# Optimization experiments

Hardware: AMD Instinct MI355X
Metric: run time of the kernel (lower is better)

## Reference

```python
import jax, jax.numpy as jnp
import numpy as np

T, B, E = 2048, 2, 1024
H, R = 16, 8
HD = E // H          # head_dim = 64
VD = E // R          # value_dim = attn_dim // num_rules = 128 (attn_dim = embed_dim)
SEL = E // H         # selection_dim = 64


def _linear_params(key, out_dim, in_dim):
    kw, kb = jax.random.split(key)
    lim = float(np.sqrt(6.0 / (in_dim + out_dim)))  # xavier_uniform
    W = jax.random.uniform(kw, (out_dim, in_dim), jnp.float32, -lim, lim)
    b = jnp.zeros((out_dim,), jnp.float32)
    return W, b


def setup_inputs() -> dict:
    key = jax.random.key(0)
    ks = jax.random.split(key, 7)
    query = jax.random.normal(ks[0], (T, B, E), jnp.float32)
    Wq, bq = _linear_params(ks[1], E, E)
    Wk, bk = _linear_params(ks[2], E, E)
    Wv, bv = _linear_params(ks[3], E, E)          # v_proj: embed_dim -> attn_dim (=E)
    Wvq, bvq = _linear_params(ks[4], SEL * H, E)  # value_q (q_compose=False)
    Wsc, bsc = _linear_params(ks[5], 1, SEL + VD) # score_network (nonlinear=False)
    Wo, bo = _linear_params(ks[6], E, H * VD)     # out_proj
    return {"query": query, "Wq": Wq, "bq": bq, "Wk": Wk, "bk": bk,
            "Wv": Wv, "bv": bv, "Wvq": Wvq, "bvq": bvq,
            "Wsc": Wsc, "bsc": bsc, "Wo": Wo, "bo": bo}


def reference(query, Wq, bq, Wk, bk, Wv, bv, Wvq, bvq, Wsc, bsc, Wo, bo):
    t, b, e = query.shape
    scaling = HD ** -0.5
    # projections (self-attention: k, v from query)
    q = (query @ Wq.T + bq) * scaling                       # (T,B,E)
    k = query @ Wk.T + bk                                   # (T,B,E)
    v = query @ Wv.T + bv                                   # (T,B,attn_dim)
    q = q.reshape(t, b, H, HD).transpose(1, 2, 0, 3)        # (B,H,T,HD)
    k = k.reshape(t, b, H, HD).transpose(1, 2, 0, 3)        # (B,H,S,HD)
    v = v.reshape(t, b, R, VD).transpose(1, 2, 0, 3)        # (B,R,S,VD)
    # standard multi-head search: softmax over source positions
    probs = jax.nn.softmax(jnp.einsum('bhtd,bhsd->bhts', q, k), axis=-1)
    # per-(head, rule) retrieved values
    attn = jnp.einsum('bhts,brsd->bhtrd', probs, v)         # (B,H,T,R,VD)
    # selection query from raw input (q_compose=False)
    v_q = (query @ Wvq.T + bvq).reshape(t, b, H, SEL).transpose(1, 2, 0, 3)  # (B,H,T,SEL)
    v_q = jnp.broadcast_to(v_q[:, :, :, None, :], (b, H, t, R, SEL))
    comp = jnp.concatenate([v_q, attn], axis=-1)            # (B,H,T,R,SEL+VD)
    score = comp @ Wsc.T + bsc                              # (B,H,T,R,1)
    sel = jax.nn.softmax(score, axis=3)                     # softmax over rules
    out = jnp.sum(attn * sel, axis=3)                       # (B,H,T,VD)
    out = out.transpose(2, 0, 1, 3).reshape(t, b, H * VD)   # (T,B,H*VD)
    return out @ Wo.T + bo                                  # (T,B,E)
```

## Files before the change

kernel.cpp:

```cpp
#include <hip/hip_runtime.h>
#include <hip/hip_bf16.h>
#include <stdint.h>

typedef unsigned short u16;
typedef unsigned int u32;
typedef __attribute__((ext_vector_type(8))) short bf16x8;
typedef __attribute__((ext_vector_type(4))) float f32x4;

#define TT 2048
#define BB 2
#define HH 16
#define RR 8
#define SS 2048
#define MROWS 4096

__device__ __forceinline__ float bf2f(u16 h){ union { u32 u; float f; } v; v.u = ((u32)h) << 16; return v.f; }
__device__ __forceinline__ u16 f2bf(float f){ union { float f; u32 u; } v; v.f = f; return (u16)((v.u + 0x7FFFu + ((v.u >> 16) & 1u)) >> 16); }
__device__ __forceinline__ void gl_lds16(const void* g, void* l){
  __builtin_amdgcn_global_load_lds((const __attribute__((address_space(1))) u32*)g,
                                   (__attribute__((address_space(3))) u32*)l, 16, 0, 0);
}

__global__ void k_cvt(const float* __restrict__ s, u16* __restrict__ d, int n, float scale){
  int i = blockIdx.x * blockDim.x + threadIdx.x;
  int st = gridDim.x * blockDim.x;
  for (; i < n; i += st) d[i] = f2bf(s[i] * scale);
}

__global__ void k_bias(const float* __restrict__ bq, const float* __restrict__ bk,
                       const float* __restrict__ bv, float* __restrict__ bb){
  int i = blockIdx.x * blockDim.x + threadIdx.x;
  if (i < 1024){ bb[i] = bq[i] * 0.125f; bb[1024 + i] = bk[i]; bb[2048 + i] = bv[i]; }
}

template<int KD, bool OBF>
__launch_bounds__(256, 2)
__global__ void k_gemm(const u16* __restrict__ A, const u16* __restrict__ Bt,
                       const float* __restrict__ bias, void* __restrict__ Cout, int ldc){
  __shared__ u16 As[128*32];
  __shared__ u16 Bs[128*32];
  const int tid = threadIdx.x, lane = tid & 63, wid = tid >> 6;
  const int mw = wid >> 1, nw = wid & 1;
  const int m0 = blockIdx.y * 128, n0 = blockIdx.x * 128;
  const f32x4 fzero = {0.f, 0.f, 0.f, 0.f};
  f32x4 acc[4][4];
  #pragma unroll
  for (int a = 0; a < 4; ++a)
    #pragma unroll
    for (int c = 0; c < 4; ++c) acc[a][c] = fzero;

  for (int k0 = 0; k0 < KD; k0 += 32){
    #pragma unroll
    for (int it = 0; it < 2; ++it){
      int c = it*256 + tid, r = c >> 2, sl = c & 3;
      gl_lds16(A + (size_t)(m0 + r)*KD + k0 + 8*(sl ^ ((r >> 1) & 3)), &As[c*8]);
    }
    #pragma unroll
    for (int it = 0; it < 2; ++it){
      int c = it*256 + tid, r = c >> 2, sl = c & 3;
      gl_lds16(Bt + (size_t)(n0 + r)*KD + k0 + 8*(sl ^ ((r >> 1) & 3)), &Bs[c*8]);
    }
    __syncthreads();
    bf16x8 af[4], bfr[4];
    #pragma unroll
    for (int mt = 0; mt < 4; ++mt){
      int r = mw*64 + mt*16 + (lane & 15);
      int pos = (lane >> 4) ^ ((r >> 1) & 3);
      af[mt] = *(const bf16x8*)&As[r*32 + pos*8];
    }
    #pragma unroll
    for (int nt = 0; nt < 4; ++nt){
      int r = nw*64 + nt*16 + (lane & 15);
      int pos = (lane >> 4) ^ ((r >> 1) & 3);
      bfr[nt] = *(const bf16x8*)&Bs[r*32 + pos*8];
    }
    #pragma unroll
    for (int mt = 0; mt < 4; ++mt)
      #pragma unroll
      for (int nt = 0; nt < 4; ++nt)
        acc[mt][nt] = __builtin_amdgcn_mfma_f32_16x16x32_bf16(af[mt], bfr[nt], acc[mt][nt], 0, 0, 0);
    __syncthreads();
  }
  #pragma unroll
  for (int nt = 0; nt < 4; ++nt){
    int col = n0 + nw*64 + nt*16 + (lane & 15);
    float bvv = bias[col];
    #pragma unroll
    for (int mt = 0; mt < 4; ++mt)
      #pragma unroll
      for (int j = 0; j < 4; ++j){
        int row = m0 + mw*64 + mt*16 + (lane >> 4)*4 + j;
        float v = acc[mt][nt][j] + bvv;
        if constexpr (OBF) ((u16*)Cout)[(size_t)row*ldc + col] = f2bf(v);
        else               ((float*)Cout)[(size_t)row*ldc + col] = v;
      }
  }
}

__global__ void k_transpose(const u16* __restrict__ qkvb, u16* __restrict__ Vt2){
  __shared__ u16 tile[32][33];
  const int b = blockIdx.z;
  const int s0 = blockIdx.x * 32, n0 = blockIdx.y * 32;
  const int tx = threadIdx.x & 31, ty = threadIdx.x >> 5;
  for (int i = ty; i < 32; i += 8)
    tile[i][tx] = qkvb[(size_t)((s0 + i)*BB + b)*3072 + 2048 + n0 + tx];
  __syncthreads();
  for (int i = ty; i < 32; i += 8){
    int c = n0 + i;
    int nr = ((c & 127) << 3) | (c >> 7);
    Vt2[(size_t)b*1024*SS + (size_t)nr*SS + s0 + tx] = tile[tx][i];
  }
}

__global__ void k_vw2(const u16* __restrict__ qkvb, const float* __restrict__ Wsc,
                      u16* __restrict__ vwa){
  int idx = blockIdx.x * blockDim.x + threadIdx.x;
  if (idx >= BB*16*SS) return;
  int s = idx & (SS - 1);
  int r = (idx >> 11) & 15;
  int b = idx >> 15;
  float a;
  if (r < 8){
    const u16* vrow = qkvb + (size_t)(s*BB + b)*3072 + 2048 + r*128;
    a = 0.f;
    #pragma unroll 8
    for (int d = 0; d < 128; ++d) a += bf2f(vrow[d]) * Wsc[64 + d];
  } else if (r == 8) a = 1.0f;
  else a = 0.f;
  vwa[(size_t)(b*16 + r)*SS + s] = f2bf(a);
}

__launch_bounds__(512, 4)
__global__ void k_attn2(const u16* __restrict__ qkvb, const u16* __restrict__ vwa,
                        u16* __restrict__ probs, float* __restrict__ selp, int bh0){
  __shared__ u16 Qs[64*64];
  __shared__ u16 Ks[128*64];
  __shared__ u16 P[64*136];
  __shared__ float pwL[8][16][16];
  const int tid = threadIdx.x, lane = tid & 63, wid = tid >> 6;
  const int bhl = blockIdx.y;
  const int bh = bh0 + bhl;
  const int t0 = blockIdx.x * 64;
  const int b = bh >> 4, h = bh & 15;
  const u16* qbase = qkvb + b*3072 + h*64;
  const u16* kbase = qkvb + b*3072 + 1024 + h*64;
  const u16* vwbase = vwa + (size_t)b*16*SS;
  u16* pbase = probs + ((size_t)bhl*TT + t0)*SS;
  const f32x4 fzero = {0.f, 0.f, 0.f, 0.f};

  {
    int c = tid, r = c >> 3, sl = c & 7;
    gl_lds16(qbase + (size_t)(t0 + r)*6144 + 8*(sl ^ (r & 7)), &Qs[c*8]);
  }
  __syncthreads();
  bf16x8 qf[4][2];
  #pragma unroll
  for (int mt = 0; mt < 4; ++mt)
    #pragma unroll
    for (int kk = 0; kk < 2; ++kk){
      int r = mt*16 + (lane & 15);
      int pos = (kk*4 + (lane >> 4)) ^ (r & 7);
      qf[mt][kk] = *(const bf16x8*)&Qs[r*64 + pos*8];
    }

  f32x4 pwacc = fzero;
  const int mtp = wid & 3, kks = (wid >> 2)*2;

  for (int s0 = 0; s0 < SS; s0 += 128){
    #pragma unroll
    for (int it = 0; it < 2; ++it){
      int c = it*512 + tid, r = c >> 3, sl = c & 7;
      gl_lds16(kbase + (size_t)(s0 + r)*6144 + 8*(sl ^ (r & 7)), &Ks[c*8]);
    }
    __syncthreads();
    bf16x8 kf[2];
    #pragma unroll
    for (int kk = 0; kk < 2; ++kk){
      int r = wid*16 + (lane & 15);
      int pos = (kk*4 + (lane >> 4)) ^ (r & 7);
      kf[kk] = *(const bf16x8*)&Ks[r*64 + pos*8];
    }
    #pragma unroll
    for (int bt = 0; bt < 4; ++bt){
      f32x4 sa = fzero;
      sa = __builtin_amdgcn_mfma_f32_16x16x32_bf16(kf[0], qf[bt][0], sa, 0, 0, 0);
      sa = __builtin_amdgcn_mfma_f32_16x16x32_bf16(kf[1], qf[bt][1], sa, 0, 0, 0);
      u32 w0 = (u32)f2bf(__expf(sa[0])) | ((u32)f2bf(__expf(sa[1])) << 16);
      u32 w1 = (u32)f2bf(__expf(sa[2])) | ((u32)f2bf(__expf(sa[3])) << 16);
      int t = bt*16 + (lane & 15);
      int sl = wid*16 + (lane >> 4)*4;
      uint2 pk; pk.x = w0; pk.y = w1;
      *(uint2*)&P[t*136 + sl] = pk;
    }
    __syncthreads();
    bf16x8 vwf[2];
    #pragma unroll
    for (int kq = 0; kq < 2; ++kq)
      vwf[kq] = *(const bf16x8*)&vwbase[(size_t)(lane & 15)*SS + s0 + (kks + kq)*32 + (lane >> 4)*8];
    #pragma unroll
    for (int kq = 0; kq < 2; ++kq){
      int kk = kks + kq;
      bf16x8 pa = *(const bf16x8*)&P[(mtp*16 + (lane & 15))*136 + kk*32 + (lane >> 4)*8];
      pwacc = __builtin_amdgcn_mfma_f32_16x16x32_bf16(pa, vwf[kq], pwacc, 0, 0, 0);
    }
    #pragma unroll
    for (int cc = 0; cc < 2; ++cc){
      int c = cc*512 + tid;
      int row = c >> 4, col = c & 15;
      bf16x8 v = *(const bf16x8*)&P[row*136 + col*8];
      *(bf16x8*)&pbase[(size_t)row*SS + s0 + col*8] = v;
    }
  }

  #pragma unroll
  for (int j = 0; j < 4; ++j)
    pwL[wid][(lane >> 4)*4 + j][lane & 15] = pwacc[j];
  __syncthreads();
  if (tid < 64){
    int mt = tid >> 4, tr = tid & 15;
    float pw[9];
    #pragma unroll
    for (int r = 0; r < 9; ++r) pw[r] = pwL[mt][tr][r] + pwL[mt + 4][tr][r];
    float rs = pw[8];
    float inv = 1.0f / rs;
    float mx = -3.0e38f;
    #pragma unroll
    for (int r = 0; r < 8; ++r) mx = fmaxf(mx, pw[r]*inv);
    float e[8], ssum = 0.f;
    #pragma unroll
    for (int r = 0; r < 8; ++r){ e[r] = __expf(pw[r]*inv - mx); ssum += e[r]; }
    #pragma unroll
    for (int r = 0; r < 8; ++r)
      selp[((size_t)bh*TT + t0 + tid)*8 + r] = e[r] / (ssum * rs);
  }
}

__launch_bounds__(512, 2)
__global__ void k_pv4(const u16* __restrict__ probs, const u16* __restrict__ Vt2,
                      const float* __restrict__ selp, u16* __restrict__ oattn,
                      int bh0, int G){
  __shared__ u16 L[4*16384];
  const int tid = threadIdx.x, lane = tid & 63, wid = tid >> 6;
  const int mw = wid & 1, nw2 = wid >> 1;
  int fid = blockIdx.x, bhl, xy;
  if (G >= 8){ bhl = (fid & 7) + 8*(fid >> 8); xy = (fid >> 3) & 31; }
  else       { bhl = fid >> 5;                 xy = fid & 31; }
  const int t0 = (xy >> 2) * 256;
  const int n0 = (xy & 3) * 256;
  const int bh = bh0 + bhl, b = bh >> 4, h = bh & 15;
  const u16* Abase = probs + ((size_t)bhl*TT + t0)*SS;
  const u16* Bbase = Vt2 + (size_t)b*1024*SS + (size_t)n0*SS;
  const f32x4 fzero = {0.f, 0.f, 0.f, 0.f};
  f32x4 acc[8][4];
  #pragma unroll
  for (int a = 0; a < 8; ++a)
    #pragma unroll
    for (int c = 0; c < 4; ++c) acc[a][c] = fzero;

  auto stage = [&](int q){
    u16* As = &L[(q & 3) * 16384];
    u16* Bs = As + 8192;
    #pragma unroll
    for (int i = 0; i < 2; ++i){
      int ci = i*512 + tid, r = ci >> 2, sl = ci & 3;
      gl_lds16(Abase + (size_t)r*SS + q*32 + 8*(sl ^ ((r >> 1) & 3)), &As[ci*8]);
    }
    #pragma unroll
    for (int i = 0; i < 2; ++i){
      int ci = i*512 + tid, r = ci >> 2, sl = ci & 3;
      gl_lds16(Bbase + (size_t)r*SS + q*32 + 8*(sl ^ ((r >> 1) & 3)), &Bs[ci*8]);
    }
  };

  stage(0); stage(1); stage(2);
  asm volatile("s_waitcnt vmcnt(8)" ::: "memory");
  __builtin_amdgcn_s_barrier();
  __builtin_amdgcn_sched_barrier(0);

  for (int q = 0; q < 64; ++q){
    const u16* As = &L[(q & 3) * 16384];
    const u16* Bs = As + 8192;
    bf16x8 af[8], bfr[4];
    #pragma unroll
    for (int mf = 0; mf < 8; ++mf){
      int r = mw*128 + mf*16 + (lane & 15);
      int pos = (lane >> 4) ^ ((r >> 1) & 3);
      af[mf] = *(const bf16x8*)&As[r*32 + pos*8];
    }
    #pragma unroll
    for (int nf = 0; nf < 4; ++nf){
      int r = nw2*64 + nf*16 + (lane & 15);
      int pos = (lane >> 4) ^ ((r >> 1) & 3);
      bfr[nf] = *(const bf16x8*)&Bs[r*32 + pos*8];
    }
    if (q + 3 < 64) stage(q + 3);
    __builtin_amdgcn_s_setprio(1);
    #pragma unroll
    for (int mf = 0; mf < 8; ++mf)
      #pragma unroll
      for (int nf = 0; nf < 4; ++nf)
        acc[mf][nf] = __builtin_amdgcn_mfma_f32_16x16x32_bf16(af[mf], bfr[nf], acc[mf][nf], 0, 0, 0);
    __builtin_amdgcn_s_setprio(0);
    if (q < 61)       asm volatile("s_waitcnt vmcnt(8)" ::: "memory");
    else if (q == 61) asm volatile("s_waitcnt vmcnt(4)" ::: "memory");
    else              asm volatile("s_waitcnt vmcnt(0)" ::: "memory");
    __builtin_amdgcn_s_barrier();
    __builtin_amdgcn_sched_barrier(0);
  }

  const int c15 = lane & 15, g = lane >> 4, r8 = c15 & 7;
  float sel[8][4];
  #pragma unroll
  for (int mf = 0; mf < 8; ++mf)
    #pragma unroll
    for (int j = 0; j < 4; ++j){
      int trow = t0 + mw*128 + mf*16 + g*4 + j;
      sel[mf][j] = selp[((size_t)bh*TT + trow)*8 + r8];
    }
  #pragma unroll
  for (int mf = 0; mf < 8; ++mf)
    #pragma unroll
    for (int nf = 0; nf < 4; ++nf){
      float v0 = acc[mf][nf][0] * sel[mf][0];
      float v1 = acc[mf][nf][1] * sel[mf][1];
      float v2 = acc[mf][nf][2] * sel[mf][2];
      float v3 = acc[mf][nf][3] * sel[mf][3];
      #pragma unroll
      for (int mask = 1; mask < 8; mask <<= 1){
        v0 += __shfl_xor(v0, mask, 64);
        v1 += __shfl_xor(v1, mask, 64);
        v2 += __shfl_xor(v2, mask, 64);
        v3 += __shfl_xor(v3, mask, 64);
      }
      if (r8 == 0){
        int dglob = (n0 >> 3) + nw2*8 + nf*2 + (c15 >> 3);
        int tb = t0 + mw*128 + mf*16 + g*4;
        u16* dst = oattn + (size_t)(tb*BB + b)*2048 + h*128 + dglob;
        dst[0*BB*2048] = f2bf(v0);
        dst[1*BB*2048] = f2bf(v1);
        dst[2*BB*2048] = f2bf(v2);
        dst[3*BB*2048] = f2bf(v3);
      }
    }
}

extern "C" void kernel_launch(void* const* d_in, const int* in_sizes, int n_in,
                              void* d_out, int out_size, void* d_ws, size_t ws_size,
                              hipStream_t stream){
  (void)in_sizes; (void)n_in;
  const float* query = (const float*)d_in[0];
  const float* Wq  = (const float*)d_in[1];
  const float* bq  = (const float*)d_in[2];
  const float* Wk  = (const float*)d_in[3];
  const float* bk  = (const float*)d_in[4];
  const float* Wv  = (const float*)d_in[5];
  const float* bv  = (const float*)d_in[6];
  const float* Wsc = (const float*)d_in[9];
  const float* Wo  = (const float*)d_in[11];
  const float* bo  = (const float*)d_in[12];

  char* p = (char*)d_ws;
  auto carve = [&](size_t bytes) -> char* {
    char* r = p; p += (bytes + 255) & ~((size_t)255); return r;
  };
  u16*   Xb     = (u16*)  carve((size_t)MROWS*1024*2);
  u16*   Wb     = (u16*)  carve((size_t)3072*1024*2);
  u16*   Wob    = (u16*)  carve((size_t)1024*2048*2);
  float* bb     = (float*)carve(3072*4);
  u16*   qkvb   = (u16*)  carve((size_t)MROWS*3072*2);
  u16*   Vt2    = (u16*)  carve((size_t)BB*1024*SS*2);
  u16*   vwa    = (u16*)  carve((size_t)BB*16*SS*2);
  u16*   oattn  = (u16*)  carve((size_t)MROWS*2048*2);
  float* selp   = (float*)carve((size_t)32*TT*RR*4);
  size_t fixed = (size_t)(p - (char*)d_ws);
  int G = 32;
  while (G > 1 && fixed + ((size_t)G*TT*SS*2 + 256) > ws_size) G >>= 1;
  u16* probs;
  if (fixed + ((size_t)G*TT*SS*2 + 256) <= ws_size){
    probs = (u16*)carve((size_t)G*TT*SS*2);
  } else {
    G = 1;
    probs = Xb;
  }

  k_cvt<<<1024, 256, 0, stream>>>(query, Xb, MROWS*1024, 1.0f);
  k_cvt<<<512, 256, 0, stream>>>(Wq, Wb, 1024*1024, 0.125f);
  k_cvt<<<512, 256, 0, stream>>>(Wk, Wb + 1024*1024, 1024*1024, 1.0f);
  k_cvt<<<512, 256, 0, stream>>>(Wv, Wb + 2*1024*1024, 1024*1024, 1.0f);
  k_cvt<<<1024, 256, 0, stream>>>(Wo, Wob, 1024*2048, 1.0f);
  k_bias<<<4, 256, 0, stream>>>(bq, bk, bv, bb);
  k_gemm<1024, true><<<dim3(24, 32), 256, 0, stream>>>(Xb, Wb, bb, qkvb, 3072);
  k_transpose<<<dim3(64, 32, 2), 256, 0, stream>>>(qkvb, Vt2);
  k_vw2<<<256, 256, 0, stream>>>(qkvb, Wsc, vwa);
  for (int bh0 = 0; bh0 < 32; bh0 += G){
    k_attn2<<<dim3(32, G), 512, 0, stream>>>(qkvb, vwa, probs, selp, bh0);
    k_pv4<<<G*32, 512, 0, stream>>>(probs, Vt2, selp, oattn, bh0, G);
  }
  k_gemm<2048, false><<<dim3(8, 32), 256, 0, stream>>>(oattn, Wob, bo, d_out, 1024);
}
```

Measured before the change: 433.5 us.

## Shrink PV GEMM tile to 256x128 and double-buffer LDS fragment reads

The probs×V kernel's per-block output tile shrinks from 256x256 to 256x128, doubling the grid and halving the per-wave accumulator footprint. The eight waves are regrouped as a 4x2 grid with 64x64 subtiles. Fragment reads for the next k-step are issued before the MFMAs of the current one, giving a software-pipelined A/B register double buffer. The intent is better occupancy and latency hiding, at the cost of loading each probs tile twice across N-blocks, which doubles A-operand traffic.

```diff
diff --git a/kernel.cpp b/kernel.cpp
--- a/kernel.cpp
+++ b/kernel.cpp
@@ -236,89 +236,101 @@
 }
 
 __launch_bounds__(512, 2)
-__global__ void k_pv4(const u16* __restrict__ probs, const u16* __restrict__ Vt2,
+__global__ void k_pv5(const u16* __restrict__ probs, const u16* __restrict__ Vt2,
                       const float* __restrict__ selp, u16* __restrict__ oattn,
                       int bh0, int G){
-  __shared__ u16 L[4*16384];
+  __shared__ u16 L[4*12288];
   const int tid = threadIdx.x, lane = tid & 63, wid = tid >> 6;
-  const int mw = wid & 1, nw2 = wid >> 1;
+  const int mw = wid >> 1, nw = wid & 1;
   int fid = blockIdx.x, bhl, xy;
-  if (G >= 8){ bhl = (fid & 7) + 8*(fid >> 8); xy = (fid >> 3) & 31; }
-  else       { bhl = fid >> 5;                 xy = fid & 31; }
-  const int t0 = (xy >> 2) * 256;
-  const int n0 = (xy & 3) * 256;
+  if (G >= 8){ bhl = (fid & 7) + 8*(fid >> 9); xy = (fid >> 3) & 63; }
+  else       { bhl = fid >> 6;                 xy = fid & 63; }
+  const int t0 = (xy >> 3) * 256;
+  const int n0 = (xy & 7) * 128;
   const int bh = bh0 + bhl, b = bh >> 4, h = bh & 15;
   const u16* Abase = probs + ((size_t)bhl*TT + t0)*SS;
   const u16* Bbase = Vt2 + (size_t)b*1024*SS + (size_t)n0*SS;
   const f32x4 fzero = {0.f, 0.f, 0.f, 0.f};
-  f32x4 acc[8][4];
-  #pragma unroll
-  for (int a = 0; a < 8; ++a)
+  f32x4 acc[4][4];
+  #pragma unroll
+  for (int a = 0; a < 4; ++a)
     #pragma unroll
     for (int c = 0; c < 4; ++c) acc[a][c] = fzero;
 
   auto stage = [&](int q){
-    u16* As = &L[(q & 3) * 16384];
+    u16* As = &L[(q & 3) * 12288];
     u16* Bs = As + 8192;
     #pragma unroll
     for (int i = 0; i < 2; ++i){
       int ci = i*512 + tid, r = ci >> 2, sl = ci & 3;
       gl_lds16(Abase + (size_t)r*SS + q*32 + 8*(sl ^ ((r >> 1) & 3)), &As[ci*8]);
     }
-    #pragma unroll
-    for (int i = 0; i < 2; ++i){
-      int ci = i*512 + tid, r = ci >> 2, sl = ci & 3;
+    {
+      int ci = tid, r = ci >> 2, sl = ci & 3;
       gl_lds16(Bbase + (size_t)r*SS + q*32 + 8*(sl ^ ((r >> 1) & 3)), &Bs[ci*8]);
     }
   };
-
-  stage(0); stage(1); stage(2);
-  asm volatile("s_waitcnt vmcnt(8)" ::: "memory");
-  __builtin_amdgcn_s_barrier();
-  __builtin_amdgcn_sched_barrier(0);
-
-  for (int q = 0; q < 64; ++q){
-    const u16* As = &L[(q & 3) * 16384];
+  auto read_frags = [&](int q, bf16x8 (&af)[4], bf16x8 (&bfr)[4]){
+    const u16* As = &L[(q & 3) * 12288];
     const u16* Bs = As + 8192;
-    bf16x8 af[8], bfr[4];
-    #pragma unroll
-    for (int mf = 0; mf < 8; ++mf){
-      int r = mw*128 + mf*16 + (lane & 15);
+    #pragma unroll
+    for (int mf = 0; mf < 4; ++mf){
+      int r = mw*64 + mf*16 + (lane & 15);
       int pos = (lane >> 4) ^ ((r >> 1) & 3);
       af[mf] = *(const bf16x8*)&As[r*32 + pos*8];
     }
     #pragma unroll
     for (int nf = 0; nf < 4; ++nf){
-      int r = nw2*64 + nf*16 + (lane & 15);
+      int r = nw*64 + nf*16 + (lane & 15);
       int pos = (lane >> 4) ^ ((r >> 1) & 3);
       bfr[nf] = *(const bf16x8*)&Bs[r*32 + pos*8];
     }
-    if (q + 3 < 64) stage(q + 3);
+  };
+  auto mfma16 = [&](bf16x8 (&af)[4], bf16x8 (&bfr)[4]){
     __builtin_amdgcn_s_setprio(1);
     #pragma unroll
-    for (int mf = 0; mf < 8; ++mf)
+    for (int mf = 0; mf < 4; ++mf)
       #pragma unroll
       for (int nf = 0; nf < 4; ++nf)
         acc[mf][nf] = __builtin_amdgcn_mfma_f32_16x16x32_bf16(af[mf], bfr[nf], acc[mf][nf], 0, 0, 0);
     __builtin_amdgcn_s_setprio(0);
-    if (q < 61)       asm volatile("s_waitcnt vmcnt(8)" ::: "memory");
-    else if (q == 61) asm volatile("s_waitcnt vmcnt(4)" ::: "memory");
-    else              asm volatile("s_waitcnt vmcnt(0)" ::: "memory");
+  };
+  auto endwait = [&](int q){
+    if (q <= 60) asm volatile("s_waitcnt vmcnt(3)" ::: "memory");
+    else         asm volatile("s_waitcnt vmcnt(0)" ::: "memory");
     __builtin_amdgcn_s_barrier();
     __builtin_amdgcn_sched_barrier(0);
+  };
+
+  bf16x8 afA[4], bfA[4], afB[4], bfB[4];
+  stage(0); stage(1); stage(2);
+  asm volatile("s_waitcnt vmcnt(3)" ::: "memory");
+  __builtin_amdgcn_s_barrier();
+  __builtin_amdgcn_sched_barrier(0);
+  read_frags(0, afA, bfA);
+
+  for (int qq = 0; qq < 64; qq += 2){
+    if (qq + 3 < 64) stage(qq + 3);
+    read_frags(qq + 1, afB, bfB);
+    mfma16(afA, bfA);
+    endwait(qq);
+    if (qq + 4 < 64) stage(qq + 4);
+    if (qq + 2 < 64) read_frags(qq + 2, afA, bfA);
+    mfma16(afB, bfB);
+    endwait(qq + 1);
   }
 
   const int c15 = lane & 15, g = lane >> 4, r8 = c15 & 7;
-  float sel[8][4];
-  #pragma unroll
-  for (int mf = 0; mf < 8; ++mf)
+  float sel[4][4];
+  #pragma unroll
+  for (int mf = 0; mf < 4; ++mf)
     #pragma unroll
     for (int j = 0; j < 4; ++j){
-      int trow = t0 + mw*128 + mf*16 + g*4 + j;
+      int trow = t0 + mw*64 + mf*16 + g*4 + j;
       sel[mf][j] = selp[((size_t)bh*TT + trow)*8 + r8];
     }
   #pragma unroll
-  for (int mf = 0; mf < 8; ++mf)
+  for (int mf = 0; mf < 4; ++mf)
     #pragma unroll
     for (int nf = 0; nf < 4; ++nf){
       float v0 = acc[mf][nf][0] * sel[mf][0];
@@ -333,8 +345,8 @@
         v3 += __shfl_xor(v3, mask, 64);
       }
       if (r8 == 0){
-        int dglob = (n0 >> 3) + nw2*8 + nf*2 + (c15 >> 3);
-        int tb = t0 + mw*128 + mf*16 + g*4;
+        int dglob = (n0 >> 3) + nw*8 + nf*2 + (c15 >> 3);
+        int tb = t0 + mw*64 + mf*16 + g*4;
         u16* dst = oattn + (size_t)(tb*BB + b)*2048 + h*128 + dglob;
         dst[0*BB*2048] = f2bf(v0);
         dst[1*BB*2048] = f2bf(v1);
@@ -394,7 +406,7 @@
   k_vw2<<<256, 256, 0, stream>>>(qkvb, Wsc, vwa);
   for (int bh0 = 0; bh0 < 32; bh0 += G){
     k_attn2<<<dim3(32, G), 512, 0, stream>>>(qkvb, vwa, probs, selp, bh0);
-    k_pv4<<<G*32, 512, 0, stream>>>(probs, Vt2, selp, oattn, bh0, G);
+    k_pv5<<<G*64, 512, 0, stream>>>(probs, Vt2, selp, oattn, bh0, G);
   }
   k_gemm<2048, false><<<dim3(8, 32), 256, 0, stream>>>(oattn, Wob, bo, d_out, 1024);
 }
```

Result: slower. 490.2 us (+13.1%).

## Restructure PV GEMM pipeline into double-buffered K=64 tiles with split-phase loads

Applied to the files above, without the earlier changes.

Replaces the four-deep ring of K=32 LDS stages in the probs×V kernel with two K=64 buffers. Each buffer is filled in four half-tile global-to-LDS loads that are interleaved with four MFMA phases, each phase covering half the N fragments. The aim is finer-grained overlap of memory traffic with matrix math while using the same LDS footprint. In exchange it adds several extra workgroup barriers per iteration and holds fewer B fragments in registers at a time.

```diff
diff --git a/kernel.cpp b/kernel.cpp
--- a/kernel.cpp
+++ b/kernel.cpp
@@ -236,10 +236,10 @@
 }
 
 __launch_bounds__(512, 2)
-__global__ void k_pv4(const u16* __restrict__ probs, const u16* __restrict__ Vt2,
+__global__ void k_pv6(const u16* __restrict__ probs, const u16* __restrict__ Vt2,
                       const float* __restrict__ selp, u16* __restrict__ oattn,
                       int bh0, int G){
-  __shared__ u16 L[4*16384];
+  __shared__ u16 L[2*32768];
   const int tid = threadIdx.x, lane = tid & 63, wid = tid >> 6;
   const int mw = wid & 1, nw2 = wid >> 1;
   int fid = blockIdx.x, bhl, xy;
@@ -257,53 +257,77 @@
     #pragma unroll
     for (int c = 0; c < 4; ++c) acc[a][c] = fzero;
 
-  auto stage = [&](int q){
-    u16* As = &L[(q & 3) * 16384];
-    u16* Bs = As + 8192;
+  auto stageH = [&](int kt, int which){
+    int isB = which & 1, subk = which >> 1;
+    u16* dst = &L[(kt & 1)*32768 + isB*16384 + subk*8192];
+    const u16* src = isB ? Bbase : Abase;
     #pragma unroll
     for (int i = 0; i < 2; ++i){
       int ci = i*512 + tid, r = ci >> 2, sl = ci & 3;
-      gl_lds16(Abase + (size_t)r*SS + q*32 + 8*(sl ^ ((r >> 1) & 3)), &As[ci*8]);
-    }
-    #pragma unroll
-    for (int i = 0; i < 2; ++i){
-      int ci = i*512 + tid, r = ci >> 2, sl = ci & 3;
-      gl_lds16(Bbase + (size_t)r*SS + q*32 + 8*(sl ^ ((r >> 1) & 3)), &Bs[ci*8]);
+      gl_lds16(src + (size_t)r*SS + kt*64 + subk*32 + 8*(sl ^ ((r >> 1) & 3)), &dst[ci*8]);
     }
   };
-
-  stage(0); stage(1); stage(2);
-  asm volatile("s_waitcnt vmcnt(8)" ::: "memory");
-  __builtin_amdgcn_s_barrier();
-  __builtin_amdgcn_sched_barrier(0);
-
-  for (int q = 0; q < 64; ++q){
-    const u16* As = &L[(q & 3) * 16384];
-    const u16* Bs = As + 8192;
-    bf16x8 af[8], bfr[4];
+  auto readA = [&](int kt, int kk, bf16x8 (&af)[8]){
+    const u16* As = &L[(kt & 1)*32768 + kk*8192];
     #pragma unroll
     for (int mf = 0; mf < 8; ++mf){
       int r = mw*128 + mf*16 + (lane & 15);
       int pos = (lane >> 4) ^ ((r >> 1) & 3);
       af[mf] = *(const bf16x8*)&As[r*32 + pos*8];
     }
-    #pragma unroll
-    for (int nf = 0; nf < 4; ++nf){
-      int r = nw2*64 + nf*16 + (lane & 15);
+  };
+  auto readB = [&](int kt, int kk, int nh, bf16x8 (&bfr)[2]){
+    const u16* Bs = &L[(kt & 1)*32768 + 16384 + kk*8192];
+    #pragma unroll
+    for (int nf = 0; nf < 2; ++nf){
+      int r = nw2*64 + nh*32 + nf*16 + (lane & 15);
       int pos = (lane >> 4) ^ ((r >> 1) & 3);
       bfr[nf] = *(const bf16x8*)&Bs[r*32 + pos*8];
     }
-    if (q + 3 < 64) stage(q + 3);
+  };
+  auto mfma16 = [&](bf16x8 (&af)[8], bf16x8 (&bfr)[2], int nh){
     __builtin_amdgcn_s_setprio(1);
     #pragma unroll
     for (int mf = 0; mf < 8; ++mf)
       #pragma unroll
-      for (int nf = 0; nf < 4; ++nf)
-        acc[mf][nf] = __builtin_amdgcn_mfma_f32_16x16x32_bf16(af[mf], bfr[nf], acc[mf][nf], 0, 0, 0);
+      for (int nf = 0; nf < 2; ++nf)
+        acc[mf][nh*2 + nf] = __builtin_amdgcn_mfma_f32_16x16x32_bf16(af[mf], bfr[nf], acc[mf][nh*2 + nf], 0, 0, 0);
     __builtin_amdgcn_s_setprio(0);
-    if (q < 61)       asm volatile("s_waitcnt vmcnt(8)" ::: "memory");
-    else if (q == 61) asm volatile("s_waitcnt vmcnt(4)" ::: "memory");
-    else              asm volatile("s_waitcnt vmcnt(0)" ::: "memory");
+  };
+
+  stageH(0, 0); stageH(0, 1); stageH(0, 2); stageH(0, 3);
+  asm volatile("s_waitcnt vmcnt(4)" ::: "memory");
+  __builtin_amdgcn_s_barrier();
+  __builtin_amdgcn_sched_barrier(0);
+
+  bf16x8 af[8], bfr[2];
+  for (int kt = 0; kt < 32; ++kt){
+    const bool last = (kt == 31);
+    readA(kt, 0, af);
+    readB(kt, 0, 0, bfr);
+    if (!last) stageH(kt + 1, 0);
+    __builtin_amdgcn_s_barrier();
+    mfma16(af, bfr, 0);
+    __builtin_amdgcn_s_barrier();
+    readB(kt, 0, 1, bfr);
+    if (!last) stageH(kt + 1, 1);
+    __builtin_amdgcn_s_barrier();
+    mfma16(af, bfr, 1);
+    if (!last) asm volatile("s_waitcnt vmcnt(4)" ::: "memory");
+    else       asm volatile("s_waitcnt vmcnt(0)" ::: "memory");
+    __builtin_amdgcn_s_barrier();
+    __builtin_amdgcn_sched_barrier(0);
+    readA(kt, 1, af);
+    readB(kt, 1, 0, bfr);
+    if (!last) stageH(kt + 1, 2);
+    __builtin_amdgcn_s_barrier();
+    mfma16(af, bfr, 0);
+    __builtin_amdgcn_s_barrier();
+    readB(kt, 1, 1, bfr);
+    if (!last) stageH(kt + 1, 3);
+    __builtin_amdgcn_s_barrier();
+    mfma16(af, bfr, 1);
+    asm volatile("s_waitcnt vmcnt(%0)" :: "i"(4) : "memory");
     __builtin_amdgcn_s_barrier();
     __builtin_amdgcn_sched_barrier(0);
   }
@@ -394,7 +418,7 @@
   k_vw2<<<256, 256, 0, stream>>>(qkvb, Wsc, vwa);
   for (int bh0 = 0; bh0 < 32; bh0 += G){
     k_attn2<<<dim3(32, G), 512, 0, stream>>>(qkvb, vwa, probs, selp, bh0);
-    k_pv4<<<G*32, 512, 0, stream>>>(probs, Vt2, selp, oattn, bh0, G);
+    k_pv6<<<G*32, 512, 0, stream>>>(probs, Vt2, selp, oattn, bh0, G);
   }
   k_gemm<2048, false><<<dim3(8, 32), 256, 0, stream>>>(oattn, Wob, bo, d_out, 1024);
 }
```

Result: no change. 432.9 us (median of 2 runs) (-0.1%).

## Load probs operand directly into registers, stage only V in LDS

Applied to the files above, without the earlier changes.

The PV kernel now reads the probability (A) fragments straight from global memory into double-buffered registers, one step ahead. Only the V (B) tiles still go through the four-deep LDS ring, which halves shared memory use and removes the A LDS reads. The waitcnt thresholds are retuned for the new mix of register and LDS loads. In exchange, the four waves that share the same A rows each fetch them separately, so global/L2 traffic for A rises and register pressure grows.

```diff
diff --git a/kernel.cpp b/kernel.cpp
--- a/kernel.cpp
+++ b/kernel.cpp
@@ -236,10 +236,10 @@
 }
 
 __launch_bounds__(512, 2)
-__global__ void k_pv4(const u16* __restrict__ probs, const u16* __restrict__ Vt2,
+__global__ void k_pv7(const u16* __restrict__ probs, const u16* __restrict__ Vt2,
                       const float* __restrict__ selp, u16* __restrict__ oattn,
                       int bh0, int G){
-  __shared__ u16 L[4*16384];
+  __shared__ u16 L[4*8192];
   const int tid = threadIdx.x, lane = tid & 63, wid = tid >> 6;
   const int mw = wid & 1, nw2 = wid >> 1;
   int fid = blockIdx.x, bhl, xy;
@@ -257,14 +257,15 @@
     #pragma unroll
     for (int c = 0; c < 4; ++c) acc[a][c] = fzero;
 
-  auto stage = [&](int q){
-    u16* As = &L[(q & 3) * 16384];
-    u16* Bs = As + 8192;
-    #pragma unroll
-    for (int i = 0; i < 2; ++i){
-      int ci = i*512 + tid, r = ci >> 2, sl = ci & 3;
-      gl_lds16(Abase + (size_t)r*SS + q*32 + 8*(sl ^ ((r >> 1) & 3)), &As[ci*8]);
-    }
+  const u16* Alane = Abase + (size_t)(mw*128 + (lane & 15))*SS + (lane >> 4)*8;
+
+  auto loadA = [&](int q, bf16x8 (&af)[8]){
+    #pragma unroll
+    for (int mf = 0; mf < 8; ++mf)
+      af[mf] = *(const bf16x8*)&Alane[(size_t)mf*16*SS + q*32];
+  };
+  auto stageB = [&](int q){
+    u16* Bs = &L[(q & 3) * 8192];
     #pragma unroll
     for (int i = 0; i < 2; ++i){
       int ci = i*512 + tid, r = ci >> 2, sl = ci & 3;
@@ -272,40 +273,41 @@
     }
   };
 
-  stage(0); stage(1); stage(2);
-  asm volatile("s_waitcnt vmcnt(8)" ::: "memory");
+  bf16x8 afA[8], afB[8];
+  loadA(0, afA);
+  stageB(0); stageB(1); stageB(2);
+  asm volatile("s_waitcnt vmcnt(4)" ::: "memory");
   __builtin_amdgcn_s_barrier();
   __builtin_amdgcn_sched_barrier(0);
 
-  for (int q = 0; q < 64; ++q){
-    const u16* As = &L[(q & 3) * 16384];
-    const u16* Bs = As + 8192;
-    bf16x8 af[8], bfr[4];
-    #pragma unroll
-    for (int mf = 0; mf < 8; ++mf){
-      int r = mw*128 + mf*16 + (lane & 15);
-      int pos = (lane >> 4) ^ ((r >> 1) & 3);
-      af[mf] = *(const bf16x8*)&As[r*32 + pos*8];
-    }
-    #pragma unroll
-    for (int nf = 0; nf < 4; ++nf){
-      int r = nw2*64 + nf*16 + (lane & 15);
-      int pos = (lane >> 4) ^ ((r >> 1) & 3);
-      bfr[nf] = *(const bf16x8*)&Bs[r*32 + pos*8];
-    }
-    if (q + 3 < 64) stage(q + 3);
-    __builtin_amdgcn_s_setprio(1);
-    #pragma unroll
-    for (int mf = 0; mf < 8; ++mf)
+  for (int qq = 0; qq < 64; qq += 2){
+    #pragma unroll
+    for (int half = 0; half < 2; ++half){
+      const int q = qq + half;
+      bf16x8* cons = half ? afB : afA;
+      bf16x8* next = half ? afA : afB;
+      const u16* Bs = &L[(q & 3) * 8192];
+      bf16x8 bfr[4];
       #pragma unroll
-      for (int nf = 0; nf < 4; ++nf)
-        acc[mf][nf] = __builtin_amdgcn_mfma_f32_16x16x32_bf16(af[mf], bfr[nf], acc[mf][nf], 0, 0, 0);
-    __builtin_amdgcn_s_setprio(0);
-    if (q < 61)       asm volatile("s_waitcnt vmcnt(8)" ::: "memory");
-    else if (q == 61) asm volatile("s_waitcnt vmcnt(4)" ::: "memory");
-    else              asm volatile("s_waitcnt vmcnt(0)" ::: "memory");
-    __builtin_amdgcn_s_barrier();
-    __builtin_amdgcn_sched_barrier(0);
+      for (int nf = 0; nf < 4; ++nf){
+        int r = nw2*64 + nf*16 + (lane & 15);
+        int pos = (lane >> 4) ^ ((r >> 1) & 3);
+        bfr[nf] = *(const bf16x8*)&Bs[r*32 + pos*8];
+      }
+      if (q + 1 < 64) loadA(q + 1, *(bf16x8(*)[8])next);
+      if (q + 3 < 64) stageB(q + 3);
+      __builtin_amdgcn_s_setprio(1);
+      #pragma unroll
+      for (int mf = 0; mf < 8; ++mf)
+        #pragma unroll
+        for (int nf = 0; nf < 4; ++nf)
+          acc[mf][nf] = __builtin_amdgcn_mfma_f32_16x16x32_bf16(cons[mf], bfr[nf], acc[mf][nf], 0, 0, 0);
+      __builtin_amdgcn_s_setprio(0);
+      if (q < 61) asm volatile("s_waitcnt vmcnt(10)" ::: "memory");
+      else        asm volatile("s_waitcnt vmcnt(8)"  ::: "memory");
+      __builtin_amdgcn_s_barrier();
+      __builtin_amdgcn_sched_barrier(0);
+    }
   }
 
   const int c15 = lane & 15, g = lane >> 4, r8 = c15 & 7;
@@ -394,7 +396,7 @@
   k_vw2<<<256, 256, 0, stream>>>(qkvb, Wsc, vwa);
   for (int bh0 = 0; bh0 < 32; bh0 += G){
     k_attn2<<<dim3(32, G), 512, 0, stream>>>(qkvb, vwa, probs, selp, bh0);
-    k_pv4<<<G*32, 512, 0, stream>>>(probs, Vt2, selp, oattn, bh0, G);
+    k_pv7<<<G*32, 512, 0, stream>>>(probs, Vt2, selp, oattn, bh0, G);
   }
   k_gemm<2048, false><<<dim3(8, 32), 256, 0, stream>>>(oattn, Wob, bo, d_out, 1024);
 }
```

Measured after the change: 777.2 us. 79.3% more time.
